# Kernel tuning notes

Measured on AMD Instinct MI355X. Metric: run time of the kernel, lower is better.

## Reference

```python
import jax, jax.numpy as jnp
import numpy as np

B, T, D, H = 64, 1024, 256, 256
MAX_MEAN = 1000.0
MAX_LOG_VAR = 30.0
HALF_LOG_2PI = 0.5 * float(np.log(2.0 * np.pi))


def _lin(k, fan_in, fan_out):
    kw, kb = jax.random.split(k)
    lim = 1.0 / np.sqrt(fan_in)
    W = jax.random.uniform(kw, (fan_in, fan_out), jnp.float32, -lim, lim)
    b = jax.random.uniform(kb, (fan_out,), jnp.float32, -lim, lim)
    return W, b


def setup_inputs() -> dict:
    key = jax.random.key(0)
    ks = jax.random.split(key, 7)
    x = jax.random.normal(ks[0], (B, T, D), jnp.float32)
    h0 = jnp.zeros((B, H), jnp.float32)
    eps = jax.random.normal(ks[1], (B, T, H), jnp.float32)
    Wz, bz = _lin(ks[2], H + D, H)          # linear_z (input order: [x, h])
    Wr, br = _lin(ks[3], H + D, H)          # linear_r
    Wtx, btx = _lin(ks[4], D, H)            # linear_h_tilda_x
    Wth, bth = _lin(ks[5], H, H)            # linear_h_tilda_h_m1
    Wd, bd = _lin(ks[6], H, 2 * H)          # distribution_params -> (mean, log_var)
    return dict(x=x, h0=h0, eps=eps, Wz=Wz, bz=bz, Wr=Wr, br=br,
                Wtx=Wtx, btx=btx, Wth=Wth, bth=bth, Wd=Wd, bd=bd)


def reference(x, h0, eps, Wz, bz, Wr, br, Wtx, btx, Wth, bth, Wd, bd):
    def step(h, inp):
        x_t, e_t = inp                                  # [B,D], [B,H]
        xh = jnp.concatenate([x_t, h], axis=-1)         # [B, D+H]
        z = jax.nn.sigmoid(xh @ Wz + bz)
        r = jax.nn.sigmoid(xh @ Wr + br)
        h_til = jnp.tanh(x_t @ Wtx + btx + r * (h @ Wth + bth))
        h_base = z * h + (1.0 - z) * h_til
        params = h_base @ Wd + bd                       # [B, 2H]
        mean, log_var = jnp.split(params, 2, axis=-1)
        mean = jnp.clip(mean, -MAX_MEAN, MAX_MEAN)
        log_var = jnp.clip(log_var, -MAX_LOG_VAR, MAX_LOG_VAR)
        std = jnp.exp(0.5 * log_var)
        sample = mean + std * e_t                       # rsample
        # Normal log_prob at its own rsample: (sample-mean)/std == e_t exactly
        log_prob = -0.5 * e_t * e_t - 0.5 * log_var - HALF_LOG_2PI
        return sample, (sample, log_prob)

    xT = jnp.swapaxes(x, 0, 1)      # [T,B,D]
    epsT = jnp.swapaxes(eps, 0, 1)  # [T,B,H]
    _, (h_seq, lp_seq) = jax.lax.scan(step, h0, (xT, epsT))
    h_ts = jnp.swapaxes(h_seq, 0, 1)                    # [B,T,H]
    return h_ts, h_ts[:, -1:, :]
```

## Files before the change

kernel.cpp:

```cpp
#include <hip/hip_runtime.h>
#include <hip/hip_bf16.h>

typedef unsigned short ushort_t;
typedef unsigned int uint_t;
typedef unsigned long long u64_t;
using f32x4 = __attribute__((ext_vector_type(4))) float;
using bf4 = __attribute__((ext_vector_type(4))) short;
using short8 = __attribute__((ext_vector_type(8))) short;

#define MFMA_B16(a,b,c) __builtin_amdgcn_mfma_f32_16x16x32_bf16((a),(b),(c),0,0,0)
#define MFMA_F8(a,b,c)  __builtin_amdgcn_mfma_f32_16x16x32_fp8_fp8((long)(a),(long)(b),(c),0,0,0)

static __device__ __forceinline__ float bf2f(ushort_t u){
  unsigned v = ((unsigned)u) << 16;
  return __builtin_bit_cast(float, v);
}
static __device__ __forceinline__ ushort_t f2bf(float f){
  __hip_bfloat16 h = __float2bfloat16(f);
  return __builtin_bit_cast(unsigned short, h);
}
static __device__ __forceinline__ f32x4 unpack4(bf4 v){
  f32x4 r;
  r[0]=bf2f((ushort_t)v[0]); r[1]=bf2f((ushort_t)v[1]);
  r[2]=bf2f((ushort_t)v[2]); r[3]=bf2f((ushort_t)v[3]);
  return r;
}
static __device__ __forceinline__ unsigned pack_fp8x4(f32x4 f){
  unsigned u = __builtin_amdgcn_cvt_pk_fp8_f32(f[0], f[1], 0, false);
  u = __builtin_amdgcn_cvt_pk_fp8_f32(f[2], f[3], u, true);
  return u;
}

#define W_ELEMS  524288
#define AUX_OFF  524288
#define AUX_BTH  768
#define AUX_BD   1024
#define AUX_H0   1536
#define FLAG_BYTE 1084416u
#define F8_OFF_BYTES  1088512u
#define AX_OFF_BYTES  (2u<<20)
#define EPS_OFF_BYTES (112u<<20)
#define ROW_ZH 768
#define ROW_RH 1024
#define ROW_TH 1280
#define ROW_D  1536

#define L_WZ    0
#define L_H16   131072
#define L_HB16  139264
#define L_H8    147456
#define L_HB8   151552
#define L_BIAS  155648
#define SMEM_REC 157184

__global__ __launch_bounds__(64) void detect_kernel(const uint_t* __restrict__ x,
                                                    uint_t* __restrict__ flag)
{
  int l = threadIdx.x;
  int cnt = 0;
  for (int i = 0; i < 8; ++i){
    uint_t w = x[i*64 + l];
    uint_t e = (w >> 7) & 0xFF;
    unsigned long long m = __ballot(e >= 100 && e <= 136);
    if (l == 0) cnt += __popcll(m);
  }
  if (l == 0) *flag = (cnt >= 256) ? 1u : 0u;
}

__global__ __launch_bounds__(256) void prep_kernel(
    const void* __restrict__ Wz, const void* __restrict__ Wr,
    const void* __restrict__ Wtx, const void* __restrict__ Wth,
    const void* __restrict__ Wd,
    const void* __restrict__ bz, const void* __restrict__ br,
    const void* __restrict__ btx, const void* __restrict__ bth,
    const void* __restrict__ bd, const void* __restrict__ h0,
    const uint_t* __restrict__ flag, ushort_t* __restrict__ o)
{
  const bool b16 = (*flag != 0);
  int i = blockIdx.x * 256 + threadIdx.x;
  const void* src; int idx;
  if (i < W_ELEMS){
    int row = i >> 8, k = i & 255;
    if      (row <  256){ src = Wz;  idx = k*256 + row;         }
    else if (row <  512){ src = Wr;  idx = k*256 + (row-256);   }
    else if (row <  768){ src = Wtx; idx = k*256 + (row-512);   }
    else if (row < 1024){ src = Wz;  idx = (256+k)*256 + (row-768);  }
    else if (row < 1280){ src = Wr;  idx = (256+k)*256 + (row-1024); }
    else if (row < 1536){ src = Wth; idx = k*256 + (row-1280);  }
    else                { src = Wd;  idx = k*512 + (row-1536);  }
  } else {
    int j = i - W_ELEMS;
    if      (j <  256){ src = bz;  idx = j;       }
    else if (j <  512){ src = br;  idx = j-256;   }
    else if (j <  768){ src = btx; idx = j-512;   }
    else if (j < 1024){ src = bth; idx = j-768;   }
    else if (j < 1536){ src = bd;  idx = j-1024;  }
    else              { src = h0;  idx = j-1536;  }
  }
  o[i] = b16 ? ((const ushort_t*)src)[idx] : f2bf(((const float*)src)[idx]);
}

__global__ __launch_bounds__(256) void prep_f8_kernel(
    const ushort_t* __restrict__ ws, unsigned char* __restrict__ o)
{
  int i = blockIdx.x * 256 + threadIdx.x;
  int m = i >> 14;
  int b = (i & 16383) * 4;
  int row = b >> 8, k = b & 255;
  int srow = (m == 0) ? (ROW_RH + row) : (m == 1) ? (ROW_TH + row) : (ROW_D + 256 + row);
  f32x4 f = unpack4(*reinterpret_cast<const bf4*>(ws + srow*256 + k));
  *reinterpret_cast<unsigned*>(o + (size_t)i*4) = pack_fp8x4(f);
}

__global__ __launch_bounds__(256) void epscvt_kernel(
    const void* __restrict__ eps, const uint_t* __restrict__ flag,
    ushort_t* __restrict__ o)
{
  const bool b16 = (*flag != 0);
  int i = blockIdx.x * 256 + threadIdx.x;
  if (b16){
    short8 v = reinterpret_cast<const short8*>(eps)[i];
    reinterpret_cast<short8*>(o)[i] = v;
  } else {
    const f32x4* e = reinterpret_cast<const f32x4*>(eps) + i*2;
    f32x4 a = e[0], b = e[1];
    short8 v;
    v[0]=(short)f2bf(a[0]); v[1]=(short)f2bf(a[1]); v[2]=(short)f2bf(a[2]); v[3]=(short)f2bf(a[3]);
    v[4]=(short)f2bf(b[0]); v[5]=(short)f2bf(b[1]); v[6]=(short)f2bf(b[2]); v[7]=(short)f2bf(b[3]);
    reinterpret_cast<short8*>(o)[i] = v;
  }
}

__global__ __launch_bounds__(256) void xproj_kernel(
    const void* __restrict__ x, const ushort_t* __restrict__ wsB,
    const ushort_t* __restrict__ aux, const uint_t* __restrict__ flag,
    ushort_t* __restrict__ Ax)
{
  __shared__ ushort_t As[32768];
  const bool b16 = (*flag != 0);
  const int tid = threadIdx.x, w = tid >> 6, l = tid & 63, lr = l & 15, lg = l >> 4;
  const int mt = blockIdx.x % 512, nb = blockIdx.x / 512;
  const int m0 = mt * 128, n0 = nb * 128;

  #pragma unroll
  for (int i = 0; i < 16; ++i){
    int gidx = i*256 + tid, row = gidx >> 5, g = gidx & 31;
    short8 v;
    if (b16){
      v = *reinterpret_cast<const short8*>((const ushort_t*)x + (m0+row)*256 + g*8);
    } else {
      const f32x4* xf = reinterpret_cast<const f32x4*>((const float*)x + (m0+row)*256 + g*8);
      f32x4 a0 = xf[0], a1 = xf[1];
      v[0]=(short)f2bf(a0[0]); v[1]=(short)f2bf(a0[1]); v[2]=(short)f2bf(a0[2]); v[3]=(short)f2bf(a0[3]);
      v[4]=(short)f2bf(a1[0]); v[5]=(short)f2bf(a1[1]); v[6]=(short)f2bf(a1[2]); v[7]=(short)f2bf(a1[3]);
    }
    *reinterpret_cast<short8*>(reinterpret_cast<char*>(As) + row*512 + ((g ^ (row&7)) << 4)) = v;
  }
  __syncthreads();

  const int wr = w >> 1, wc = w & 1;
  f32x4 acc[4][4];
  #pragma unroll
  for (int a = 0; a < 4; ++a)
    #pragma unroll
    for (int b = 0; b < 4; ++b) acc[a][b] = (f32x4){0.f,0.f,0.f,0.f};

  #pragma unroll
  for (int ks = 0; ks < 8; ++ks){
    short8 av[4], bv[4];
    #pragma unroll
    for (int mi = 0; mi < 4; ++mi){
      int rT = 64*wr + 16*mi + lr, g = ks*4 + lg;
      av[mi] = *reinterpret_cast<const short8*>(reinterpret_cast<const char*>(As) + rT*512 + ((g ^ (rT&7)) << 4));
    }
    #pragma unroll
    for (int ni = 0; ni < 4; ++ni){
      int nr = n0 + 64*wc + 16*ni + lr;
      bv[ni] = *reinterpret_cast<const short8*>(wsB + nr*256 + ks*32 + lg*8);
    }
    #pragma unroll
    for (int mi = 0; mi < 4; ++mi)
      #pragma unroll
      for (int ni = 0; ni < 4; ++ni)
        acc[mi][ni] = MFMA_B16(av[mi], bv[ni], acc[mi][ni]);
  }

  #pragma unroll
  for (int ni = 0; ni < 4; ++ni){
    int c = n0 + 64*wc + 16*ni + lr;
    float bias = bf2f(aux[c]);
    #pragma unroll
    for (int mi = 0; mi < 4; ++mi)
      #pragma unroll
      for (int j = 0; j < 4; ++j){
        int m = m0 + 64*wr + 16*mi + lg*4 + j;
        Ax[m*768 + c] = f2bf(acc[mi][ni][j] + bias);
      }
  }
}

__global__ __attribute__((amdgpu_flat_work_group_size(512, 512),
                          amdgpu_waves_per_eu(2, 2)))
void gru_kernel(
    const ushort_t* __restrict__ ws16, const unsigned char* __restrict__ f8w,
    const ushort_t* __restrict__ Ax, const ushort_t* __restrict__ eps16,
    const uint_t* __restrict__ flag, void* __restrict__ outp)
{
  extern __shared__ char smem[];
  const bool b16 = (*flag != 0);
  ushort_t* o16 = (ushort_t*)outp;
  float*    o32 = (float*)outp;
  const ushort_t* aux = ws16 + AUX_OFF;
  ushort_t* bias_lds = (ushort_t*)(smem + L_BIAS);
  const int tid = threadIdx.x, w = tid >> 6, l = tid & 63, lr = l & 15, lg = l >> 4;
  const int b0 = blockIdx.x * 16;
  const int c0 = 32 * w;
  const int cl = c0 + lg*4;

  for (int gi = tid; gi < 8192; gi += 512){
    int row = gi >> 5, g = gi & 31;
    short8 v = *reinterpret_cast<const short8*>(ws16 + (ROW_ZH + row)*256 + g*8);
    *reinterpret_cast<short8*>(smem + row*512 + ((g ^ (row&15)) << 4)) = v;
  }
  if (tid < 256) bias_lds[tid] = aux[AUX_BTH + tid];
  if (tid < 512) bias_lds[256 + tid] = aux[AUX_BD + tid];

  const unsigned char* f_rh = f8w;
  const unsigned char* f_th = f8w + 65536;
  const unsigned char* f_dl = f8w + 131072;
  u64_t wrh8[2][8], wth8[2][8], wdl8[2][8];
  short8 wdm[2][8];
  #pragma unroll
  for (int nt = 0; nt < 2; ++nt){
    int r = c0 + 16*nt + lr;
    #pragma unroll
    for (int ks = 0; ks < 8; ++ks){
      wrh8[nt][ks] = *reinterpret_cast<const u64_t*>(f_rh + r*256 + ks*32 + lg*8);
      wth8[nt][ks] = *reinterpret_cast<const u64_t*>(f_th + r*256 + ks*32 + lg*8);
      wdl8[nt][ks] = *reinterpret_cast<const u64_t*>(f_dl + r*256 + ks*32 + lg*8);
      wdm[nt][ks]  = *reinterpret_cast<const short8*>(ws16 + (ROW_D + r)*256 + ks*32 + lg*8);
    }
  }

  f32x4 hreg[2];
  #pragma unroll
  for (int nt = 0; nt < 2; ++nt){
    int c = cl + 16*nt, g = c >> 3;
    hreg[nt] = unpack4(*reinterpret_cast<const bf4*>(aux + AUX_H0 + (b0+lr)*256 + c));
    bf4 hv;
    hv[0]=(short)f2bf(hreg[nt][0]); hv[1]=(short)f2bf(hreg[nt][1]);
    hv[2]=(short)f2bf(hreg[nt][2]); hv[3]=(short)f2bf(hreg[nt][3]);
    *reinterpret_cast<bf4*>(smem + L_H16 + lr*512 + ((g ^ (lr&15)) << 4) + (c&7)*2) = hv;
    *reinterpret_cast<unsigned*>(smem + L_H8 + lr*256 + ((g ^ (lr&15)) << 3) + (c&7)) = pack_fp8x4(hreg[nt]);
  }
  __syncthreads();

  const ushort_t* apt = Ax    + (size_t)(b0+lr)*1024*768 + cl;
  const ushort_t* ept = eps16 + (size_t)(b0+lr)*1024*256 + cl;
  size_t obase = (size_t)(b0+lr)*262144 + cl;

  for (int t = 0; t < 1024; ++t){
    bf4 axzp[2], axrp[2], axtp[2], epsp[2];
    #pragma unroll
    for (int nt = 0; nt < 2; ++nt){
      axzp[nt] = *reinterpret_cast<const bf4*>(apt + 16*nt);
      axrp[nt] = *reinterpret_cast<const bf4*>(apt + 256 + 16*nt);
      axtp[nt] = *reinterpret_cast<const bf4*>(apt + 512 + 16*nt);
      epsp[nt] = *reinterpret_cast<const bf4*>(ept + 16*nt);
    }

    f32x4 az[2], ar[2], at[2];
    az[0] = (f32x4){0.f,0.f,0.f,0.f}; az[1] = az[0];
    ar[0] = az[0]; ar[1] = az[0];
    at[0] = unpack4(*reinterpret_cast<const bf4*>(bias_lds + cl));
    at[1] = unpack4(*reinterpret_cast<const bf4*>(bias_lds + cl + 16));
    #pragma unroll
    for (int ks = 0; ks < 8; ++ks){
      const int g = ks*4 + lg;
      short8 hB = *reinterpret_cast<const short8*>(smem + L_H16 + lr*512 + ((g ^ (lr&15)) << 4));
      u64_t  h8 = *reinterpret_cast<const u64_t*>(smem + L_H8 + lr*256 + ((g ^ (lr&15)) << 3));
      int nc0 = c0 + lr, nc1 = c0 + 16 + lr;
      short8 wz0 = *reinterpret_cast<const short8*>(smem + nc0*512 + ((g ^ (nc0&15)) << 4));
      short8 wz1 = *reinterpret_cast<const short8*>(smem + nc1*512 + ((g ^ (nc1&15)) << 4));
      az[0] = MFMA_B16(wz0, hB, az[0]);        az[1] = MFMA_B16(wz1, hB, az[1]);
      ar[0] = MFMA_F8(wrh8[0][ks], h8, ar[0]); ar[1] = MFMA_F8(wrh8[1][ks], h8, ar[1]);
      at[0] = MFMA_F8(wth8[0][ks], h8, at[0]); at[1] = MFMA_F8(wth8[1][ks], h8, at[1]);
    }

    #pragma unroll
    for (int nt = 0; nt < 2; ++nt){
      f32x4 axz = unpack4(axzp[nt]), axr = unpack4(axrp[nt]), axt = unpack4(axtp[nt]);
      f32x4 hb;
      bf4 hb4;
      #pragma unroll
      for (int q = 0; q < 4; ++q){
        float zp = az[nt][q] + axz[q];
        float rp = ar[nt][q] + axr[q];
        float zv = 1.f/(1.f + __expf(-zp));
        float rv = 1.f/(1.f + __expf(-rp));
        float tp = axt[q] + rv*at[nt][q];
        float e2 = __expf(-2.f*fabsf(tp));
        float tv = (1.f - e2)/(1.f + e2);
        tv = (tp < 0.f) ? -tv : tv;
        hb[q] = zv*hreg[nt][q] + (1.f - zv)*tv;
        hb4[q] = (short)f2bf(hb[q]);
      }
      int c = cl + 16*nt, g = c >> 3;
      *reinterpret_cast<bf4*>(smem + L_HB16 + lr*512 + ((g ^ (lr&15)) << 4) + (c&7)*2) = hb4;
      *reinterpret_cast<unsigned*>(smem + L_HB8 + lr*256 + ((g ^ (lr&15)) << 3) + (c&7)) = pack_fp8x4(hb);
    }
    asm volatile("s_waitcnt lgkmcnt(0)" ::: "memory");
    __builtin_amdgcn_s_barrier();
    asm volatile("" ::: "memory");

    f32x4 apm[2], apl[2];
    apm[0] = unpack4(*reinterpret_cast<const bf4*>(bias_lds + 256 + cl));
    apm[1] = unpack4(*reinterpret_cast<const bf4*>(bias_lds + 256 + cl + 16));
    apl[0] = unpack4(*reinterpret_cast<const bf4*>(bias_lds + 512 + cl));
    apl[1] = unpack4(*reinterpret_cast<const bf4*>(bias_lds + 512 + cl + 16));
    #pragma unroll
    for (int ks = 0; ks < 8; ++ks){
      const int g = ks*4 + lg;
      short8 hbB = *reinterpret_cast<const short8*>(smem + L_HB16 + lr*512 + ((g ^ (lr&15)) << 4));
      u64_t  hb8 = *reinterpret_cast<const u64_t*>(smem + L_HB8 + lr*256 + ((g ^ (lr&15)) << 3));
      apm[0] = MFMA_B16(wdm[0][ks], hbB, apm[0]); apm[1] = MFMA_B16(wdm[1][ks], hbB, apm[1]);
      apl[0] = MFMA_F8(wdl8[0][ks], hb8, apl[0]); apl[1] = MFMA_F8(wdl8[1][ks], hb8, apl[1]);
    }

    #pragma unroll
    for (int nt = 0; nt < 2; ++nt){
      f32x4 epsv = unpack4(epsp[nt]);
      bf4 s4;
      f32x4 sf;
      #pragma unroll
      for (int q = 0; q < 4; ++q){
        float mean = fminf(fmaxf(apm[nt][q], -1000.f), 1000.f);
        float lvv  = fminf(fmaxf(apl[nt][q], -30.f),   30.f);
        float s = mean + __expf(0.5f*lvv)*epsv[q];
        hreg[nt][q] = s;
        sf[q] = s;
        s4[q] = (short)f2bf(s);
      }
      int c = cl + 16*nt, g = c >> 3;
      *reinterpret_cast<bf4*>(smem + L_H16 + lr*512 + ((g ^ (lr&15)) << 4) + (c&7)*2) = s4;
      *reinterpret_cast<unsigned*>(smem + L_H8 + lr*256 + ((g ^ (lr&15)) << 3) + (c&7)) = pack_fp8x4(sf);
      size_t oi = obase + 16*nt;
      if (b16){
        *reinterpret_cast<bf4*>(o16 + oi) = s4;
        if (t == 1023) *reinterpret_cast<bf4*>(o16 + 16777216u + (size_t)(b0+lr)*256 + c) = s4;
      } else {
        *reinterpret_cast<f32x4*>(o32 + oi) = sf;
        if (t == 1023) *reinterpret_cast<f32x4*>(o32 + 16777216u + (size_t)(b0+lr)*256 + c) = sf;
      }
    }
    asm volatile("s_waitcnt lgkmcnt(0)" ::: "memory");
    __builtin_amdgcn_s_barrier();
    asm volatile("" ::: "memory");

    apt += 768; ept += 256; obase += 256;
  }
}

extern "C" void kernel_launch(void* const* d_in, const int* in_sizes, int n_in,
                              void* d_out, int out_size, void* d_ws, size_t ws_size,
                              hipStream_t stream)
{
  const void* x   = d_in[0];
  const void* h0  = d_in[1];
  const void* eps = d_in[2];
  const void* Wz  = d_in[3];
  const void* bz  = d_in[4];
  const void* Wr  = d_in[5];
  const void* br  = d_in[6];
  const void* Wtx = d_in[7];
  const void* btx = d_in[8];
  const void* Wth = d_in[9];
  const void* bth = d_in[10];
  const void* Wd  = d_in[11];
  const void* bd  = d_in[12];
  ushort_t* ws16 = (ushort_t*)d_ws;
  uint_t* flag = (uint_t*)((char*)d_ws + FLAG_BYTE);
  const ushort_t* aux = ws16 + AUX_OFF;
  unsigned char* f8w = (unsigned char*)d_ws + F8_OFF_BYTES;
  ushort_t* Ax = (ushort_t*)((char*)d_ws + AX_OFF_BYTES);
  ushort_t* eps16 = (ushort_t*)((char*)d_ws + EPS_OFF_BYTES);

  detect_kernel<<<dim3(1), dim3(64), 0, stream>>>((const uint_t*)x, flag);
  prep_kernel<<<dim3(2118), dim3(256), 0, stream>>>(Wz, Wr, Wtx, Wth, Wd,
                                                    bz, br, btx, bth, bd, h0,
                                                    flag, ws16);
  prep_f8_kernel<<<dim3(192), dim3(256), 0, stream>>>(ws16, f8w);
  epscvt_kernel<<<dim3(8192), dim3(256), 0, stream>>>(eps, flag, eps16);
  xproj_kernel<<<dim3(3072), dim3(256), 0, stream>>>(x, ws16, aux, flag, Ax);

  (void)hipFuncSetAttribute(reinterpret_cast<const void*>(&gru_kernel),
                            hipFuncAttributeMaxDynamicSharedMemorySize, SMEM_REC);
  gru_kernel<<<dim3(4), dim3(512), SMEM_REC, stream>>>(ws16, f8w, Ax, eps16, flag, d_out);
}
```

Before: 4.506 ms.

## Split GRU recurrence over 16 waves per block and use fast reciprocals

The recurrent kernel now launches 1024 threads per block instead of 512. Each wave owns 16 output columns instead of 32, which halves the per-wave MFMA chain, register-resident weights and per-step elementwise work. This shortens the latency-bound serial critical path of each timestep. Exact divisions in the sigmoid and tanh are replaced with hardware approximate reciprocals. In exchange there are more waves to synchronise at each barrier, and occupancy and register limits change because the waves_per_eu hint is dropped.

Result: slower. 8.519 ms (+89.1%).

```diff
diff --git a/kernel.cpp b/kernel.cpp
--- a/kernel.cpp
+++ b/kernel.cpp
@@ -29,6 +29,9 @@
   unsigned u = __builtin_amdgcn_cvt_pk_fp8_f32(f[0], f[1], 0, false);
   u = __builtin_amdgcn_cvt_pk_fp8_f32(f[2], f[3], u, true);
   return u;
+}
+static __device__ __forceinline__ float frcp(float x){
+  return __builtin_amdgcn_rcpf(x);
 }
 
 #define W_ELEMS  524288
@@ -199,8 +202,7 @@
   }
 }
 
-__global__ __attribute__((amdgpu_flat_work_group_size(512, 512),
-                          amdgpu_waves_per_eu(2, 2)))
+__global__ __attribute__((amdgpu_flat_work_group_size(1024, 1024)))
 void gru_kernel(
     const ushort_t* __restrict__ ws16, const unsigned char* __restrict__ f8w,
     const ushort_t* __restrict__ Ax, const ushort_t* __restrict__ eps16,
@@ -214,10 +216,10 @@
   ushort_t* bias_lds = (ushort_t*)(smem + L_BIAS);
   const int tid = threadIdx.x, w = tid >> 6, l = tid & 63, lr = l & 15, lg = l >> 4;
   const int b0 = blockIdx.x * 16;
-  const int c0 = 32 * w;
+  const int c0 = 16 * w;
   const int cl = c0 + lg*4;
 
-  for (int gi = tid; gi < 8192; gi += 512){
+  for (int gi = tid; gi < 8192; gi += 1024){
     int row = gi >> 5, g = gi & 31;
     short8 v = *reinterpret_cast<const short8*>(ws16 + (ROW_ZH + row)*256 + g*8);
     *reinterpret_cast<short8*>(smem + row*512 + ((g ^ (row&15)) << 4)) = v;
@@ -228,30 +230,28 @@
   const unsigned char* f_rh = f8w;
   const unsigned char* f_th = f8w + 65536;
   const unsigned char* f_dl = f8w + 131072;
-  u64_t wrh8[2][8], wth8[2][8], wdl8[2][8];
-  short8 wdm[2][8];
-  #pragma unroll
-  for (int nt = 0; nt < 2; ++nt){
-    int r = c0 + 16*nt + lr;
+  u64_t wrh8[8], wth8[8], wdl8[8];
+  short8 wdm[8];
+  {
+    int r = c0 + lr;
     #pragma unroll
     for (int ks = 0; ks < 8; ++ks){
-      wrh8[nt][ks] = *reinterpret_cast<const u64_t*>(f_rh + r*256 + ks*32 + lg*8);
-      wth8[nt][ks] = *reinterpret_cast<const u64_t*>(f_th + r*256 + ks*32 + lg*8);
-      wdl8[nt][ks] = *reinterpret_cast<const u64_t*>(f_dl + r*256 + ks*32 + lg*8);
-      wdm[nt][ks]  = *reinterpret_cast<const short8*>(ws16 + (ROW_D + r)*256 + ks*32 + lg*8);
-    }
-  }
-
-  f32x4 hreg[2];
-  #pragma unroll
-  for (int nt = 0; nt < 2; ++nt){
-    int c = cl + 16*nt, g = c >> 3;
-    hreg[nt] = unpack4(*reinterpret_cast<const bf4*>(aux + AUX_H0 + (b0+lr)*256 + c));
+      wrh8[ks] = *reinterpret_cast<const u64_t*>(f_rh + r*256 + ks*32 + lg*8);
+      wth8[ks] = *reinterpret_cast<const u64_t*>(f_th + r*256 + ks*32 + lg*8);
+      wdl8[ks] = *reinterpret_cast<const u64_t*>(f_dl + r*256 + ks*32 + lg*8);
+      wdm[ks]  = *reinterpret_cast<const short8*>(ws16 + (ROW_D + r)*256 + ks*32 + lg*8);
+    }
+  }
+
+  f32x4 hreg;
+  {
+    int c = cl, g = c >> 3;
+    hreg = unpack4(*reinterpret_cast<const bf4*>(aux + AUX_H0 + (b0+lr)*256 + c));
     bf4 hv;
-    hv[0]=(short)f2bf(hreg[nt][0]); hv[1]=(short)f2bf(hreg[nt][1]);
-    hv[2]=(short)f2bf(hreg[nt][2]); hv[3]=(short)f2bf(hreg[nt][3]);
+    hv[0]=(short)f2bf(hreg[0]); hv[1]=(short)f2bf(hreg[1]);
+    hv[2]=(short)f2bf(hreg[2]); hv[3]=(short)f2bf(hreg[3]);
     *reinterpret_cast<bf4*>(smem + L_H16 + lr*512 + ((g ^ (lr&15)) << 4) + (c&7)*2) = hv;
-    *reinterpret_cast<unsigned*>(smem + L_H8 + lr*256 + ((g ^ (lr&15)) << 3) + (c&7)) = pack_fp8x4(hreg[nt]);
+    *reinterpret_cast<unsigned*>(smem + L_H8 + lr*256 + ((g ^ (lr&15)) << 3) + (c&7)) = pack_fp8x4(hreg);
   }
   __syncthreads();
 
@@ -260,52 +260,44 @@
   size_t obase = (size_t)(b0+lr)*262144 + cl;
 
   for (int t = 0; t < 1024; ++t){
-    bf4 axzp[2], axrp[2], axtp[2], epsp[2];
-    #pragma unroll
-    for (int nt = 0; nt < 2; ++nt){
-      axzp[nt] = *reinterpret_cast<const bf4*>(apt + 16*nt);
-      axrp[nt] = *reinterpret_cast<const bf4*>(apt + 256 + 16*nt);
-      axtp[nt] = *reinterpret_cast<const bf4*>(apt + 512 + 16*nt);
-      epsp[nt] = *reinterpret_cast<const bf4*>(ept + 16*nt);
-    }
-
-    f32x4 az[2], ar[2], at[2];
-    az[0] = (f32x4){0.f,0.f,0.f,0.f}; az[1] = az[0];
-    ar[0] = az[0]; ar[1] = az[0];
-    at[0] = unpack4(*reinterpret_cast<const bf4*>(bias_lds + cl));
-    at[1] = unpack4(*reinterpret_cast<const bf4*>(bias_lds + cl + 16));
+    bf4 axzp = *reinterpret_cast<const bf4*>(apt);
+    bf4 axrp = *reinterpret_cast<const bf4*>(apt + 256);
+    bf4 axtp = *reinterpret_cast<const bf4*>(apt + 512);
+    bf4 epsp = *reinterpret_cast<const bf4*>(ept);
+
+    f32x4 az = (f32x4){0.f,0.f,0.f,0.f};
+    f32x4 ar = az;
+    f32x4 at = unpack4(*reinterpret_cast<const bf4*>(bias_lds + cl));
     #pragma unroll
     for (int ks = 0; ks < 8; ++ks){
       const int g = ks*4 + lg;
       short8 hB = *reinterpret_cast<const short8*>(smem + L_H16 + lr*512 + ((g ^ (lr&15)) << 4));
       u64_t  h8 = *reinterpret_cast<const u64_t*>(smem + L_H8 + lr*256 + ((g ^ (lr&15)) << 3));
-      int nc0 = c0 + lr, nc1 = c0 + 16 + lr;
-      short8 wz0 = *reinterpret_cast<const short8*>(smem + nc0*512 + ((g ^ (nc0&15)) << 4));
-      short8 wz1 = *reinterpret_cast<const short8*>(smem + nc1*512 + ((g ^ (nc1&15)) << 4));
-      az[0] = MFMA_B16(wz0, hB, az[0]);        az[1] = MFMA_B16(wz1, hB, az[1]);
-      ar[0] = MFMA_F8(wrh8[0][ks], h8, ar[0]); ar[1] = MFMA_F8(wrh8[1][ks], h8, ar[1]);
-      at[0] = MFMA_F8(wth8[0][ks], h8, at[0]); at[1] = MFMA_F8(wth8[1][ks], h8, at[1]);
-    }
-
-    #pragma unroll
-    for (int nt = 0; nt < 2; ++nt){
-      f32x4 axz = unpack4(axzp[nt]), axr = unpack4(axrp[nt]), axt = unpack4(axtp[nt]);
+      int nc = c0 + lr;
+      short8 wz = *reinterpret_cast<const short8*>(smem + nc*512 + ((g ^ (nc&15)) << 4));
+      az = MFMA_B16(wz, hB, az);
+      ar = MFMA_F8(wrh8[ks], h8, ar);
+      at = MFMA_F8(wth8[ks], h8, at);
+    }
+
+    {
+      f32x4 axz = unpack4(axzp), axr = unpack4(axrp), axt = unpack4(axtp);
       f32x4 hb;
       bf4 hb4;
       #pragma unroll
       for (int q = 0; q < 4; ++q){
-        float zp = az[nt][q] + axz[q];
-        float rp = ar[nt][q] + axr[q];
-        float zv = 1.f/(1.f + __expf(-zp));
-        float rv = 1.f/(1.f + __expf(-rp));
-        float tp = axt[q] + rv*at[nt][q];
+        float zp = az[q] + axz[q];
+        float rp = ar[q] + axr[q];
+        float zv = frcp(1.f + __expf(-zp));
+        float rv = frcp(1.f + __expf(-rp));
+        float tp = axt[q] + rv*at[q];
         float e2 = __expf(-2.f*fabsf(tp));
-        float tv = (1.f - e2)/(1.f + e2);
+        float tv = (1.f - e2) * frcp(1.f + e2);
         tv = (tp < 0.f) ? -tv : tv;
-        hb[q] = zv*hreg[nt][q] + (1.f - zv)*tv;
+        hb[q] = zv*hreg[q] + (1.f - zv)*tv;
         hb4[q] = (short)f2bf(hb[q]);
       }
-      int c = cl + 16*nt, g = c >> 3;
+      int c = cl, g = c >> 3;
       *reinterpret_cast<bf4*>(smem + L_HB16 + lr*512 + ((g ^ (lr&15)) << 4) + (c&7)*2) = hb4;
       *reinterpret_cast<unsigned*>(smem + L_HB8 + lr*256 + ((g ^ (lr&15)) << 3) + (c&7)) = pack_fp8x4(hb);
     }
@@ -313,43 +305,38 @@
     __builtin_amdgcn_s_barrier();
     asm volatile("" ::: "memory");
 
-    f32x4 apm[2], apl[2];
-    apm[0] = unpack4(*reinterpret_cast<const bf4*>(bias_lds + 256 + cl));
-    apm[1] = unpack4(*reinterpret_cast<const bf4*>(bias_lds + 256 + cl + 16));
-    apl[0] = unpack4(*reinterpret_cast<const bf4*>(bias_lds + 512 + cl));
-    apl[1] = unpack4(*reinterpret_cast<const bf4*>(bias_lds + 512 + cl + 16));
+    f32x4 apm = unpack4(*reinterpret_cast<const bf4*>(bias_lds + 256 + cl));
+    f32x4 apl = unpack4(*reinterpret_cast<const bf4*>(bias_lds + 512 + cl));
     #pragma unroll
     for (int ks = 0; ks < 8; ++ks){
       const int g = ks*4 + lg;
       short8 hbB = *reinterpret_cast<const short8*>(smem + L_HB16 + lr*512 + ((g ^ (lr&15)) << 4));
       u64_t  hb8 = *reinterpret_cast<const u64_t*>(smem + L_HB8 + lr*256 + ((g ^ (lr&15)) << 3));
-      apm[0] = MFMA_B16(wdm[0][ks], hbB, apm[0]); apm[1] = MFMA_B16(wdm[1][ks], hbB, apm[1]);
-      apl[0] = MFMA_F8(wdl8[0][ks], hb8, apl[0]); apl[1] = MFMA_F8(wdl8[1][ks], hb8, apl[1]);
-    }
-
-    #pragma unroll
-    for (int nt = 0; nt < 2; ++nt){
-      f32x4 epsv = unpack4(epsp[nt]);
+      apm = MFMA_B16(wdm[ks], hbB, apm);
+      apl = MFMA_F8(wdl8[ks], hb8, apl);
+    }
+
+    {
+      f32x4 epsv = unpack4(epsp);
       bf4 s4;
       f32x4 sf;
       #pragma unroll
       for (int q = 0; q < 4; ++q){
-        float mean = fminf(fmaxf(apm[nt][q], -1000.f), 1000.f);
-        float lvv  = fminf(fmaxf(apl[nt][q], -30.f),   30.f);
+        float mean = fminf(fmaxf(apm[q], -1000.f), 1000.f);
+        float lvv  = fminf(fmaxf(apl[q], -30.f),   30.f);
         float s = mean + __expf(0.5f*lvv)*epsv[q];
-        hreg[nt][q] = s;
+        hreg[q] = s;
         sf[q] = s;
         s4[q] = (short)f2bf(s);
       }
-      int c = cl + 16*nt, g = c >> 3;
+      int c = cl, g = c >> 3;
       *reinterpret_cast<bf4*>(smem + L_H16 + lr*512 + ((g ^ (lr&15)) << 4) + (c&7)*2) = s4;
       *reinterpret_cast<unsigned*>(smem + L_H8 + lr*256 + ((g ^ (lr&15)) << 3) + (c&7)) = pack_fp8x4(sf);
-      size_t oi = obase + 16*nt;
       if (b16){
-        *reinterpret_cast<bf4*>(o16 + oi) = s4;
+        *reinterpret_cast<bf4*>(o16 + obase) = s4;
         if (t == 1023) *reinterpret_cast<bf4*>(o16 + 16777216u + (size_t)(b0+lr)*256 + c) = s4;
       } else {
-        *reinterpret_cast<f32x4*>(o32 + oi) = sf;
+        *reinterpret_cast<f32x4*>(o32 + obase) = sf;
         if (t == 1023) *reinterpret_cast<f32x4*>(o32 + 16777216u + (size_t)(b0+lr)*256 + c) = sf;
       }
     }
@@ -395,5 +382,5 @@
 
   (void)hipFuncSetAttribute(reinterpret_cast<const void*>(&gru_kernel),
                             hipFuncAttributeMaxDynamicSharedMemorySize, SMEM_REC);
-  gru_kernel<<<dim3(4), dim3(512), SMEM_REC, stream>>>(ws16, f8w, Ax, eps16, flag, d_out);
-}
+  gru_kernel<<<dim3(4), dim3(1024), SMEM_REC, stream>>>(ws16, f8w, Ax, eps16, flag, d_out);
+}
```
